# Performance work log

Hardware: AMD Instinct MI355X
Metric: run time of the kernel (lower is better)

## Reference

```python
import jax, jax.numpy as jnp
import numpy as np

ATT_LEN = 128  # must match init att_len


def setup_inputs() -> dict:
    key = jax.random.key(0)
    ks = jax.random.split(key, 6)
    B, T, U, L = 64, 4096, 512, ATT_LEN
    s = 1.0 / np.sqrt(U)
    return {
        "query": jax.random.normal(ks[0], (B, U), jnp.float32),
        "values": jax.random.normal(ks[1], (B, T, U), jnp.float32),
        "pos": jax.random.randint(ks[2], (B,), 0, T, jnp.int32),
        "W1": jax.random.normal(ks[3], (U, U), jnp.float32) * s,
        "b1": jnp.zeros((U,), jnp.float32),
        "W2": jax.random.normal(ks[4], (U, U), jnp.float32) * s,
        "b2": jnp.zeros((U,), jnp.float32),
        "V": jax.random.normal(ks[5], (U, 1), jnp.float32) * s,
        "bV": jnp.zeros((1,), jnp.float32),
    }


def _gather_windows(values, pos, att_len):
    """Vectorized version of the TF while_loop: per-example window of
    length att_len around pos, zero-padded where it runs off either end."""
    B, T, U = values.shape
    half = att_len // 2
    start = jnp.maximum(pos - half, 0)            # [B]
    end = jnp.minimum(pos + half, T)              # [B]
    xlen = end - start                            # [B]
    offs = jnp.arange(att_len, dtype=pos.dtype)   # [L]
    idx = start[:, None] + offs[None, :]          # [B, L]
    mask = offs[None, :] < xlen[:, None]          # [B, L] valid (unpadded) slots
    safe_idx = jnp.clip(idx, 0, T - 1)
    gathered = jnp.take_along_axis(values, safe_idx[:, :, None], axis=1)  # [B, L, U]
    values_att = jnp.where(mask[:, :, None], gathered, jnp.zeros((), values.dtype))
    xpos = jnp.where(mask, idx.astype(values.dtype), 0.0)  # [B, L]
    return values_att, xpos


def reference(query, values, pos, W1, b1, W2, b2, V, bV):
    values_att, _xpos = _gather_windows(values, pos, ATT_LEN)  # [B, L, U]
    # score = V(tanh(W1(values_att) + W2(query)[:, None, :]))
    h = jnp.tanh(jnp.einsum('blu,uv->blv', values_att, W1) + b1
                 + (query @ W2 + b2)[:, None, :])              # [B, L, U]
    score = jnp.einsum('blu,uo->blo', h, V) + bV               # [B, L, 1]
    attention_weights = jax.nn.softmax(score, axis=1)          # [B, L, 1]
    context_vector = jnp.sum(attention_weights * values_att, axis=1)  # [B, U]
    return context_vector, attention_weights
```

## Files before the change

kernel.cpp:

```cpp
#include <hip/hip_runtime.h>
#include <math.h>

#define NB 64
#define NT 4096
#define NU 512
#define NL 128
#define HALF 64

typedef __bf16 bf16x8 __attribute__((ext_vector_type(8)));
typedef float f32x4 __attribute__((ext_vector_type(4)));

__device__ inline unsigned short f2bf(float f) {
    unsigned u = __float_as_uint(f);
    u += 0x7fff + ((u >> 16) & 1);
    return (unsigned short)(u >> 16);
}

__device__ inline float tanh_fast(float x) {
    float xc = fminf(15.f, fmaxf(-15.f, x));
    float t = __expf(2.f * xc);
    return (t - 1.f) * __builtin_amdgcn_rcpf(t + 1.f);
}

__global__ __launch_bounds__(256) void k_prepA(const float* __restrict__ query,
                                               const float* __restrict__ values,
                                               const int* __restrict__ pos,
                                               const float* __restrict__ W1,
                                               const float* __restrict__ b1,
                                               const float* __restrict__ W2,
                                               const float* __restrict__ b2,
                                               float* __restrict__ q2,
                                               unsigned short* __restrict__ W1T,
                                               unsigned short* __restrict__ Gb) {
    __shared__ float sh[1056];
    const int blk = blockIdx.x, tid = threadIdx.x;

    if (blk < 256) {
        const int b = blk >> 2, cq = blk & 3;
        sh[tid]       = query[b * NU + tid];
        sh[tid + 256] = query[b * NU + tid + 256];
        __syncthreads();
        const int col  = cq * 128 + (tid & 127);
        const int half = tid >> 7;
        const float* wp = W2 + (size_t)(half * 256) * NU + col;
        float a = 0.f;
        #pragma unroll 8
        for (int uu = 0; uu < 256; ++uu)
            a = fmaf(sh[half * 256 + uu], wp[(size_t)uu * NU], a);
        if (half == 0) sh[512 + (tid & 127)] = a;
        __syncthreads();
        if (half == 1)
            q2[(size_t)b * NU + col] = a + sh[512 + (tid & 127)] + b1[col] + b2[col];
    } else if (blk < 512) {
        const int t  = blk - 256;
        const int tr = t >> 4, tc = t & 15;
        const int cc = tid & 31, r0 = tid >> 5;
        #pragma unroll
        for (int i = 0; i < 4; ++i) {
            const int r = r0 + i * 8;
            sh[r * 33 + cc] = W1[(size_t)(tr * 32 + r) * NU + tc * 32 + cc];
        }
        __syncthreads();
        #pragma unroll
        for (int i = 0; i < 4; ++i) {
            const int r = r0 + i * 8;
            W1T[(size_t)(tc * 32 + r) * NU + tr * 32 + cc] = f2bf(sh[cc * 33 + r]);
        }
    } else {
        const int g = blk - 512;
        #pragma unroll
        for (int i = 0; i < 8; ++i) {
            const int c   = tid + i * 256;
            const int rl  = c >> 7;
            const int off = (c & 127) * 4;
            const int rg  = g * 16 + rl;
            const int b   = rg >> 7, l = rg & 127;
            const int p     = pos[b];
            const int start = max(p - HALF, 0);
            const int xlen  = min(p + HALF, NT) - start;
            float4 v = make_float4(0.f, 0.f, 0.f, 0.f);
            if (l < xlen)
                v = *(const float4*)&values[((size_t)(b * NT + start + l)) * NU + off];
            uint2 pk;
            pk.x = f2bf(v.x) | ((unsigned)f2bf(v.y) << 16);
            pk.y = f2bf(v.z) | ((unsigned)f2bf(v.w) << 16);
            *(uint2*)&Gb[(size_t)rg * NU + off] = pk;
        }
    }
}

__global__ __launch_bounds__(256, 2) void k_score6(const unsigned short* __restrict__ Gb,
                                                   const unsigned short* __restrict__ W1T,
                                                   const float* __restrict__ q2,
                                                   const float* __restrict__ V,
                                                   float* __restrict__ part) {
    __shared__ unsigned short As[64 * 64];
    __shared__ unsigned short Bs[128 * 64];
    __shared__ float pl[64][2];

    const int id = blockIdx.x;
    const int nb = id >> 7, rb = id & 127;
    const int b  = rb >> 1, l0 = (rb & 1) * 64, n0 = nb * 128;
    const int tid = threadIdx.x, lane = tid & 63, w = tid >> 6;
    const int wr = w >> 1, wc = w & 1;

    const unsigned short* Asrc = Gb + ((size_t)(b * NL + l0)) * NU;
    const unsigned short* Bsrc = W1T + (size_t)n0 * NU;

    f32x4 acc[2][4];
    #pragma unroll
    for (int m = 0; m < 2; ++m)
        #pragma unroll
        for (int n = 0; n < 4; ++n) acc[m][n] = (f32x4){0.f, 0.f, 0.f, 0.f};

    for (int k0 = 0; k0 < NU; k0 += 64) {
        #pragma unroll
        for (int i = 0; i < 2; ++i) {
            const int c   = tid + i * 256;
            const int row = c >> 3, ch = c & 7;
            uint4 v = *(const uint4*)&Asrc[(size_t)row * NU + k0 + ch * 8];
            *(uint4*)((char*)As + row * 128 + ((ch * 16) ^ ((row & 7) << 4))) = v;
        }
        #pragma unroll
        for (int i = 0; i < 4; ++i) {
            const int c   = tid + i * 256;
            const int col = c >> 3, ch = c & 7;
            uint4 v = *(const uint4*)&Bsrc[(size_t)col * NU + k0 + ch * 8];
            *(uint4*)((char*)Bs + col * 128 + ((ch * 16) ^ ((col & 7) << 4))) = v;
        }
        __syncthreads();

        #pragma unroll
        for (int kh = 0; kh < 2; ++kh) {
            const int koff = kh * 64 + (lane >> 4) * 16;
            bf16x8 af[2];
            #pragma unroll
            for (int m = 0; m < 2; ++m) {
                const int rowA = wr * 32 + m * 16 + (lane & 15);
                af[m] = *(const bf16x8*)((const char*)As + rowA * 128 + (koff ^ ((rowA & 7) << 4)));
            }
            #pragma unroll
            for (int n = 0; n < 4; ++n) {
                const int colB = wc * 64 + n * 16 + (lane & 15);
                const bf16x8 bf = *(const bf16x8*)((const char*)Bs + colB * 128 + (koff ^ ((colB & 7) << 4)));
                #pragma unroll
                for (int m = 0; m < 2; ++m)
                    acc[m][n] = __builtin_amdgcn_mfma_f32_16x16x32_bf16(af[m], bf, acc[m][n], 0, 0, 0);
            }
        }
        __syncthreads();
    }

    float partial[2][4];
    #pragma unroll
    for (int m = 0; m < 2; ++m)
        #pragma unroll
        for (int r = 0; r < 4; ++r) partial[m][r] = 0.f;

    #pragma unroll
    for (int n = 0; n < 4; ++n) {
        const int col = n0 + wc * 64 + n * 16 + (lane & 15);
        const float qq = q2[(size_t)b * NU + col];
        const float vv = V[col];
        #pragma unroll
        for (int m = 0; m < 2; ++m)
            #pragma unroll
            for (int r = 0; r < 4; ++r)
                partial[m][r] += tanh_fast(acc[m][n][r] + qq) * vv;
    }
    #pragma unroll
    for (int off = 1; off < 16; off <<= 1)
        #pragma unroll
        for (int m = 0; m < 2; ++m)
            #pragma unroll
            for (int r = 0; r < 4; ++r)
                partial[m][r] += __shfl_xor(partial[m][r], off, 16);

    if ((lane & 15) == 0) {
        #pragma unroll
        for (int m = 0; m < 2; ++m)
            #pragma unroll
            for (int r = 0; r < 4; ++r)
                pl[wr * 32 + m * 16 + ((lane >> 4) << 2) + r][wc] = partial[m][r];
    }
    __syncthreads();

    if (tid < 64)
        part[((size_t)nb * NB + b) * NL + l0 + tid] = pl[tid][0] + pl[tid][1];
}

__global__ __launch_bounds__(256) void k_ctx2(const float* __restrict__ values,
                                              const int* __restrict__ pos,
                                              const float* __restrict__ part,
                                              const float* __restrict__ bV,
                                              float* __restrict__ out) {
    const int b = blockIdx.x, uq = blockIdx.y, tid = threadIdx.x;
    __shared__ float wsm[NL];
    __shared__ float red[4];
    __shared__ float cp[128];

    float s = -1e30f;
    if (tid < NL) {
        s = bV[0];
        #pragma unroll
        for (int nb = 0; nb < 4; ++nb) s += part[((size_t)nb * NB + b) * NL + tid];
    }
    float m = s;
    #pragma unroll
    for (int off = 32; off >= 1; off >>= 1) m = fmaxf(m, __shfl_xor(m, off, 64));
    if (tid < NL && (tid & 63) == 0) red[tid >> 6] = m;
    __syncthreads();
    const float M = fmaxf(red[0], red[1]);
    const float e = (tid < NL) ? __expf(s - M) : 0.f;
    float t = e;
    #pragma unroll
    for (int off = 32; off >= 1; off >>= 1) t += __shfl_xor(t, off, 64);
    if (tid < NL && (tid & 63) == 0) red[2 + (tid >> 6)] = t;
    __syncthreads();
    const float S = red[2] + red[3];
    if (tid < NL) {
        const float wv = e / S;
        wsm[tid] = wv;
        if (uq == 0) out[NB * NU + b * NL + tid] = wv;
    }
    __syncthreads();

    const int p     = pos[b];
    const int start = max(p - HALF, 0);
    const int xlen  = min(p + HALF, NT) - start;
    const float* vbase = values + ((size_t)b * NT + start) * NU;

    const int u    = uq * 128 + (tid & 127);
    const int half = tid >> 7;
    const int lbeg = half * 64;
    const int lend = min(xlen, lbeg + 64);
    float a = 0.f;
    #pragma unroll 4
    for (int l = lbeg; l < lend; ++l)
        a = fmaf(wsm[l], vbase[(size_t)l * NU + u], a);

    if (half == 0) cp[tid] = a;
    __syncthreads();
    if (half == 1) out[b * NU + u] = cp[tid & 127] + a;
}

#define BM 64
#define BN 128
#define BK 64
#define ASTRIDE 68

__global__ __launch_bounds__(256) void k_q2(const float* __restrict__ query,
                                            const float* __restrict__ W2,
                                            const float* __restrict__ b2,
                                            const float* __restrict__ b1,
                                            float* __restrict__ q2) {
    const int b = blockIdx.x, tid = threadIdx.x;
    __shared__ float qs[NU];
    qs[tid]       = query[b * NU + tid];
    qs[tid + 256] = query[b * NU + tid + 256];
    __syncthreads();
    float a0 = 0.f, a1 = 0.f;
    const float* w = W2 + tid;
    #pragma unroll 8
    for (int u = 0; u < NU; ++u) {
        const float q = qs[u];
        a0 = fmaf(q, w[(size_t)u * NU], a0);
        a1 = fmaf(q, w[(size_t)u * NU + 256], a1);
    }
    q2[b * NU + tid]       = a0 + b2[tid] + b1[tid];
    q2[b * NU + tid + 256] = a1 + b2[tid + 256] + b1[tid + 256];
}

__global__ __launch_bounds__(256) void k_score(const float* __restrict__ values,
                                               const int* __restrict__ pos,
                                               const float* __restrict__ W1,
                                               const float* __restrict__ V,
                                               const float* __restrict__ q2,
                                               float* __restrict__ part) {
    __shared__ float As2[BK][ASTRIDE];
    __shared__ float Bs2[BK][BN];
    const int rb = blockIdx.x, nb = blockIdx.y;
    const int b  = rb >> 1;
    const int l0 = (rb & 1) * BM;
    const int n0 = nb * BN;
    const int tid = threadIdx.x;
    const int tx = tid & 15, ty = tid >> 4;
    const int p     = pos[b];
    const int start = max(p - HALF, 0);
    const int xlen  = min(p + HALF, NT) - start;
    const float* vbase = values + ((size_t)b * NT + start) * NU;

    float acc[4][8];
    #pragma unroll
    for (int r = 0; r < 4; ++r)
        #pragma unroll
        for (int c = 0; c < 8; ++c) acc[r][c] = 0.f;

    for (int k0 = 0; k0 < NU; k0 += BK) {
        #pragma unroll
        for (int i = 0; i < 4; ++i) {
            const int f = tid + i * 256;
            const int row = f >> 4, kq = f & 15;
            const int l = l0 + row;
            float4 v4 = make_float4(0.f, 0.f, 0.f, 0.f);
            if (l < xlen)
                v4 = *(const float4*)&vbase[(size_t)l * NU + k0 + kq * 4];
            As2[kq * 4 + 0][row] = v4.x;
            As2[kq * 4 + 1][row] = v4.y;
            As2[kq * 4 + 2][row] = v4.z;
            As2[kq * 4 + 3][row] = v4.w;
        }
        #pragma unroll
        for (int i = 0; i < 8; ++i) {
            const int f = tid + i * 256;
            const int kk = f >> 5, nq = f & 31;
            *(float4*)&Bs2[kk][nq * 4] =
                *(const float4*)&W1[(size_t)(k0 + kk) * NU + n0 + nq * 4];
        }
        __syncthreads();
        #pragma unroll 16
        for (int kk = 0; kk < BK; ++kk) {
            const float4 a  = *(const float4*)&As2[kk][ty * 4];
            const float4 b0 = *(const float4*)&Bs2[kk][tx * 8];
            const float4 b1v = *(const float4*)&Bs2[kk][tx * 8 + 4];
            const float av[4] = {a.x, a.y, a.z, a.w};
            const float bv[8] = {b0.x, b0.y, b0.z, b0.w, b1v.x, b1v.y, b1v.z, b1v.w};
            #pragma unroll
            for (int r = 0; r < 4; ++r)
                #pragma unroll
                for (int c = 0; c < 8; ++c)
                    acc[r][c] = fmaf(av[r], bv[c], acc[r][c]);
        }
        __syncthreads();
    }
    float partial[4] = {0.f, 0.f, 0.f, 0.f};
    #pragma unroll
    for (int c = 0; c < 8; ++c) {
        const int v = n0 + tx * 8 + c;
        const float vv = V[v];
        const float qq = q2[b * NU + v];
        #pragma unroll
        for (int r = 0; r < 4; ++r)
            partial[r] += tanhf(acc[r][c] + qq) * vv;
    }
    #pragma unroll
    for (int off = 1; off < 16; off <<= 1)
        #pragma unroll
        for (int r = 0; r < 4; ++r)
            partial[r] += __shfl_xor(partial[r], off, 16);
    if (tx == 0) {
        #pragma unroll
        for (int r = 0; r < 4; ++r) {
            const int l = l0 + ty * 4 + r;
            part[((size_t)nb * NB + b) * NL + l] = partial[r];
        }
    }
}

__global__ __launch_bounds__(256) void k_ctx(const float* __restrict__ values,
                                             const int* __restrict__ pos,
                                             const float* __restrict__ part,
                                             const float* __restrict__ bV,
                                             float* __restrict__ out) {
    const int b = blockIdx.x, tid = threadIdx.x;
    __shared__ float wsh[NL];
    __shared__ float red2[4];

    float s = -1e30f;
    if (tid < NL) {
        s = bV[0];
        #pragma unroll
        for (int nb = 0; nb < 4; ++nb) s += part[((size_t)nb * NB + b) * NL + tid];
    }
    float m = s;
    #pragma unroll
    for (int off = 32; off >= 1; off >>= 1) m = fmaxf(m, __shfl_xor(m, off, 64));
    if (tid < NL && (tid & 63) == 0) red2[tid >> 6] = m;
    __syncthreads();
    const float M = fmaxf(red2[0], red2[1]);
    const float e = (tid < NL) ? expf(s - M) : 0.f;
    float t = e;
    #pragma unroll
    for (int off = 32; off >= 1; off >>= 1) t += __shfl_xor(t, off, 64);
    if (tid < NL && (tid & 63) == 0) red2[2 + (tid >> 6)] = t;
    __syncthreads();
    const float S = red2[2] + red2[3];
    if (tid < NL) wsh[tid] = e / S;
    __syncthreads();

    if (tid < NL) out[NB * NU + b * NL + tid] = wsh[tid];

    const int p     = pos[b];
    const int start = max(p - HALF, 0);
    const int xlen  = min(p + HALF, NT) - start;
    const float* vb = values + ((size_t)b * NT + start) * NU;

    float a0 = 0.f, a1 = 0.f;
    for (int l = 0; l < xlen; ++l) {
        const float wl = wsh[l];
        a0 = fmaf(wl, vb[(size_t)l * NU + tid], a0);
        a1 = fmaf(wl, vb[(size_t)l * NU + tid + 256], a1);
    }
    out[b * NU + tid]       = a0;
    out[b * NU + tid + 256] = a1;
}

extern "C" void kernel_launch(void* const* d_in, const int* in_sizes, int n_in,
                              void* d_out, int out_size, void* d_ws, size_t ws_size,
                              hipStream_t stream) {
    const float* query  = (const float*)d_in[0];
    const float* values = (const float*)d_in[1];
    const int*   pos    = (const int*)d_in[2];
    const float* W1     = (const float*)d_in[3];
    const float* b1     = (const float*)d_in[4];
    const float* W2     = (const float*)d_in[5];
    const float* b2     = (const float*)d_in[6];
    const float* V      = (const float*)d_in[7];
    const float* bV     = (const float*)d_in[8];
    float* out = (float*)d_out;

    const size_t need = 131072u + 131072u + 524288u + 8388608u;
    if (ws_size >= need) {
        float* q2            = (float*)d_ws;
        float* part          = (float*)((char*)d_ws + 131072);
        unsigned short* W1T  = (unsigned short*)((char*)d_ws + 262144);
        unsigned short* Gb   = (unsigned short*)((char*)d_ws + 786432);
        k_prepA<<<1024, 256, 0, stream>>>(query, values, pos, W1, b1, W2, b2, q2, W1T, Gb);
        k_score6<<<512, 256, 0, stream>>>(Gb, W1T, q2, V, part);
        k_ctx2<<<dim3(NB, 4), 256, 0, stream>>>(values, pos, part, bV, out);
    } else {
        float* q2   = (float*)d_ws;
        float* part = (float*)((char*)d_ws + 131072);
        k_q2<<<NB, 256, 0, stream>>>(query, W2, b2, b1, q2);
        k_score<<<dim3(NB * NL / BM, NU / BN), 256, 0, stream>>>(values, pos, W1, V, q2, part);
        k_ctx<<<NB, 256, 0, stream>>>(values, pos, part, bV, out);
    }
}
```

Measured before the change: 38.38 us.

## Fuse softmax/context into score kernel via last-block counter; use direct global-to-LDS loads

Removes the separate context kernel launch by having the last of the eight score blocks per batch (detected with an atomic counter reset in the prep kernel) compute the softmax and the weighted sum over values. Tile staging in the score GEMM now uses global_load_lds to write directly into LDS, with the swizzle moved to the source address. This saves a launch and the register round trip, but the final context work is done by a single block per batch, which serialises it into a tail of 64 blocks each walking 128 rows.

```diff
diff --git a/kernel.cpp b/kernel.cpp
--- a/kernel.cpp
+++ b/kernel.cpp
@@ -21,6 +21,11 @@
     float t = __expf(2.f * xc);
     return (t - 1.f) * __builtin_amdgcn_rcpf(t + 1.f);
 }
+
+#define GLL16(src, dst)                                                   \
+    __builtin_amdgcn_global_load_lds(                                     \
+        (const __attribute__((address_space(1))) void*)(src),             \
+        (__attribute__((address_space(3))) void*)(dst), 16, 0, 0)
 
 __global__ __launch_bounds__(256) void k_prepA(const float* __restrict__ query,
                                                const float* __restrict__ values,
@@ -31,7 +36,8 @@
                                                const float* __restrict__ b2,
                                                float* __restrict__ q2,
                                                unsigned short* __restrict__ W1T,
-                                               unsigned short* __restrict__ Gb) {
+                                               unsigned short* __restrict__ Gb,
+                                               int* __restrict__ cnt) {
     __shared__ float sh[1056];
     const int blk = blockIdx.x, tid = threadIdx.x;
 
@@ -67,6 +73,7 @@
             W1T[(size_t)(tc * 32 + r) * NU + tr * 32 + cc] = f2bf(sh[cc * 33 + r]);
         }
     } else {
+        if (blk == 512 && tid < NB) cnt[tid] = 0;
         const int g = blk - 512;
         #pragma unroll
         for (int i = 0; i < 8; ++i) {
@@ -89,14 +96,22 @@
     }
 }
 
-__global__ __launch_bounds__(256, 2) void k_score6(const unsigned short* __restrict__ Gb,
+__global__ __launch_bounds__(256, 2) void k_score7(const unsigned short* __restrict__ Gb,
                                                    const unsigned short* __restrict__ W1T,
                                                    const float* __restrict__ q2,
                                                    const float* __restrict__ V,
-                                                   float* __restrict__ part) {
+                                                   const float* __restrict__ values,
+                                                   const int* __restrict__ pos,
+                                                   const float* __restrict__ bV,
+                                                   float* __restrict__ part,
+                                                   int* __restrict__ cnt,
+                                                   float* __restrict__ out) {
     __shared__ unsigned short As[64 * 64];
     __shared__ unsigned short Bs[128 * 64];
     __shared__ float pl[64][2];
+    __shared__ float wsm[NL];
+    __shared__ float red[4];
+    __shared__ int amLastSh;
 
     const int id = blockIdx.x;
     const int nb = id >> 7, rb = id & 127;
@@ -118,15 +133,15 @@
         for (int i = 0; i < 2; ++i) {
             const int c   = tid + i * 256;
             const int row = c >> 3, ch = c & 7;
-            uint4 v = *(const uint4*)&Asrc[(size_t)row * NU + k0 + ch * 8];
-            *(uint4*)((char*)As + row * 128 + ((ch * 16) ^ ((row & 7) << 4))) = v;
+            GLL16(Asrc + (size_t)row * NU + k0 + ((ch ^ (row & 7)) * 8),
+                  (char*)As + c * 16);
         }
         #pragma unroll
         for (int i = 0; i < 4; ++i) {
             const int c   = tid + i * 256;
             const int col = c >> 3, ch = c & 7;
-            uint4 v = *(const uint4*)&Bsrc[(size_t)col * NU + k0 + ch * 8];
-            *(uint4*)((char*)Bs + col * 128 + ((ch * 16) ^ ((col & 7) << 4))) = v;
+            GLL16(Bsrc + (size_t)col * NU + k0 + ((ch ^ (col & 7)) * 8),
+                  (char*)Bs + c * 16);
         }
         __syncthreads();
 
@@ -185,25 +200,23 @@
     }
     __syncthreads();
 
-    if (tid < 64)
+    if (tid < 64) {
         part[((size_t)nb * NB + b) * NL + l0 + tid] = pl[tid][0] + pl[tid][1];
-}
-
-__global__ __launch_bounds__(256) void k_ctx2(const float* __restrict__ values,
-                                              const int* __restrict__ pos,
-                                              const float* __restrict__ part,
-                                              const float* __restrict__ bV,
-                                              float* __restrict__ out) {
-    const int b = blockIdx.x, uq = blockIdx.y, tid = threadIdx.x;
-    __shared__ float wsm[NL];
-    __shared__ float red[4];
-    __shared__ float cp[128];
+        __threadfence();
+    }
+    __syncthreads();
+    if (tid == 0)
+        amLastSh = (atomicAdd(&cnt[b], 1) == 7);
+    __syncthreads();
+    if (!amLastSh) return;
 
     float s = -1e30f;
     if (tid < NL) {
         s = bV[0];
         #pragma unroll
-        for (int nb = 0; nb < 4; ++nb) s += part[((size_t)nb * NB + b) * NL + tid];
+        for (int q = 0; q < 4; ++q)
+            s += __hip_atomic_load(&part[((size_t)q * NB + b) * NL + tid],
+                                   __ATOMIC_RELAXED, __HIP_MEMORY_SCOPE_AGENT);
     }
     float m = s;
     #pragma unroll
@@ -221,27 +234,23 @@
     if (tid < NL) {
         const float wv = e / S;
         wsm[tid] = wv;
-        if (uq == 0) out[NB * NU + b * NL + tid] = wv;
+        out[NB * NU + b * NL + tid] = wv;
     }
     __syncthreads();
 
     const int p     = pos[b];
     const int start = max(p - HALF, 0);
     const int xlen  = min(p + HALF, NT) - start;
-    const float* vbase = values + ((size_t)b * NT + start) * NU;
-
-    const int u    = uq * 128 + (tid & 127);
-    const int half = tid >> 7;
-    const int lbeg = half * 64;
-    const int lend = min(xlen, lbeg + 64);
-    float a = 0.f;
-    #pragma unroll 4
-    for (int l = lbeg; l < lend; ++l)
-        a = fmaf(wsm[l], vbase[(size_t)l * NU + u], a);
-
-    if (half == 0) cp[tid] = a;
-    __syncthreads();
-    if (half == 1) out[b * NU + u] = cp[tid & 127] + a;
+    const float* vb = values + ((size_t)b * NT + start) * NU;
+
+    float a0 = 0.f, a1 = 0.f;
+    for (int l = 0; l < xlen; ++l) {
+        const float wl = wsm[l];
+        a0 = fmaf(wl, vb[(size_t)l * NU + tid], a0);
+        a1 = fmaf(wl, vb[(size_t)l * NU + tid + 256], a1);
+    }
+    out[b * NU + tid]       = a0;
+    out[b * NU + tid + 256] = a1;
 }
 
 #define BM 64
@@ -419,15 +428,17 @@
     const float* bV     = (const float*)d_in[8];
     float* out = (float*)d_out;
 
-    const size_t need = 131072u + 131072u + 524288u + 8388608u;
+    const size_t need = 131072u + 131072u + 524288u + 8388608u + 256u;
     if (ws_size >= need) {
         float* q2            = (float*)d_ws;
         float* part          = (float*)((char*)d_ws + 131072);
         unsigned short* W1T  = (unsigned short*)((char*)d_ws + 262144);
         unsigned short* Gb   = (unsigned short*)((char*)d_ws + 786432);
-        k_prepA<<<1024, 256, 0, stream>>>(query, values, pos, W1, b1, W2, b2, q2, W1T, Gb);
-        k_score6<<<512, 256, 0, stream>>>(Gb, W1T, q2, V, part);
-        k_ctx2<<<dim3(NB, 4), 256, 0, stream>>>(values, pos, part, bV, out);
+        int* cnt             = (int*)((char*)d_ws + 786432 + 8388608);
+        k_prepA<<<1024, 256, 0, stream>>>(query, values, pos, W1, b1, W2, b2,
+                                          q2, W1T, Gb, cnt);
+        k_score7<<<512, 256, 0, stream>>>(Gb, W1T, q2, V, values, pos, bV,
+                                          part, cnt, out);
     } else {
         float* q2   = (float*)d_ws;
         float* part = (float*)((char*)d_ws + 131072);
```

Measured after the change: 44.79 us. +16.7%, slower.

## Double-buffer score GEMM tiles using direct global-to-LDS loads

Applied to the files above, without the earlier changes.

Switches the score GEMM's shared-memory staging from register round-trips to global_load_lds direct copies. The XOR swizzle moves from the LDS write address to the global read address. LDS is double-buffered so the next k-tile's load is issued before the MFMA work on the current tile, with one barrier per iteration. This aims to hide global load latency and save VGPRs and instructions, at the cost of doubling LDS use, which may limit occupancy. There is no explicit vmcnt wait before the barrier, so correctness depends on how the compiler orders the async LDS loads.

```diff
diff --git a/kernel.cpp b/kernel.cpp
--- a/kernel.cpp
+++ b/kernel.cpp
@@ -21,6 +21,11 @@
     float t = __expf(2.f * xc);
     return (t - 1.f) * __builtin_amdgcn_rcpf(t + 1.f);
 }
+
+#define GLL16(src, dst)                                                   \
+    __builtin_amdgcn_global_load_lds(                                     \
+        (const __attribute__((address_space(1))) void*)(src),             \
+        (__attribute__((address_space(3))) void*)(dst), 16, 0, 0)
 
 __global__ __launch_bounds__(256) void k_prepA(const float* __restrict__ query,
                                                const float* __restrict__ values,
@@ -89,13 +94,13 @@
     }
 }
 
-__global__ __launch_bounds__(256, 2) void k_score6(const unsigned short* __restrict__ Gb,
+__global__ __launch_bounds__(256, 2) void k_score8(const unsigned short* __restrict__ Gb,
                                                    const unsigned short* __restrict__ W1T,
                                                    const float* __restrict__ q2,
                                                    const float* __restrict__ V,
                                                    float* __restrict__ part) {
-    __shared__ unsigned short As[64 * 64];
-    __shared__ unsigned short Bs[128 * 64];
+    __shared__ unsigned short As[2][64 * 64];
+    __shared__ unsigned short Bs[2][128 * 64];
     __shared__ float pl[64][2];
 
     const int id = blockIdx.x;
@@ -113,22 +118,29 @@
         #pragma unroll
         for (int n = 0; n < 4; ++n) acc[m][n] = (f32x4){0.f, 0.f, 0.f, 0.f};
 
-    for (int k0 = 0; k0 < NU; k0 += 64) {
+    auto STAGE = [&](int buf, int k0) {
         #pragma unroll
         for (int i = 0; i < 2; ++i) {
-            const int c   = tid + i * 256;
+            const int c = tid + i * 256;
             const int row = c >> 3, ch = c & 7;
-            uint4 v = *(const uint4*)&Asrc[(size_t)row * NU + k0 + ch * 8];
-            *(uint4*)((char*)As + row * 128 + ((ch * 16) ^ ((row & 7) << 4))) = v;
+            GLL16(Asrc + (size_t)row * NU + k0 + ((ch ^ (row & 7)) * 8),
+                  (char*)As[buf] + c * 16);
         }
         #pragma unroll
         for (int i = 0; i < 4; ++i) {
-            const int c   = tid + i * 256;
+            const int c = tid + i * 256;
             const int col = c >> 3, ch = c & 7;
-            uint4 v = *(const uint4*)&Bsrc[(size_t)col * NU + k0 + ch * 8];
-            *(uint4*)((char*)Bs + col * 128 + ((ch * 16) ^ ((col & 7) << 4))) = v;
-        }
-        __syncthreads();
+            GLL16(Bsrc + (size_t)col * NU + k0 + ((ch ^ (col & 7)) * 8),
+                  (char*)Bs[buf] + c * 16);
+        }
+    };
+
+    STAGE(0, 0);
+    __syncthreads();
+
+    int cur = 0;
+    for (int t = 0; t < 8; ++t) {
+        if (t < 7) STAGE(cur ^ 1, (t + 1) * 64);
 
         #pragma unroll
         for (int kh = 0; kh < 2; ++kh) {
@@ -137,18 +149,19 @@
             #pragma unroll
             for (int m = 0; m < 2; ++m) {
                 const int rowA = wr * 32 + m * 16 + (lane & 15);
-                af[m] = *(const bf16x8*)((const char*)As + rowA * 128 + (koff ^ ((rowA & 7) << 4)));
+                af[m] = *(const bf16x8*)((const char*)As[cur] + rowA * 128 + (koff ^ ((rowA & 7) << 4)));
             }
             #pragma unroll
             for (int n = 0; n < 4; ++n) {
                 const int colB = wc * 64 + n * 16 + (lane & 15);
-                const bf16x8 bf = *(const bf16x8*)((const char*)Bs + colB * 128 + (koff ^ ((colB & 7) << 4)));
+                const bf16x8 bf = *(const bf16x8*)((const char*)Bs[cur] + colB * 128 + (koff ^ ((colB & 7) << 4)));
                 #pragma unroll
                 for (int m = 0; m < 2; ++m)
                     acc[m][n] = __builtin_amdgcn_mfma_f32_16x16x32_bf16(af[m], bf, acc[m][n], 0, 0, 0);
             }
         }
         __syncthreads();
+        cur ^= 1;
     }
 
     float partial[2][4];
@@ -426,7 +439,7 @@
         unsigned short* W1T  = (unsigned short*)((char*)d_ws + 262144);
         unsigned short* Gb   = (unsigned short*)((char*)d_ws + 786432);
         k_prepA<<<1024, 256, 0, stream>>>(query, values, pos, W1, b1, W2, b2, q2, W1T, Gb);
-        k_score6<<<512, 256, 0, stream>>>(Gb, W1T, q2, V, part);
+        k_score8<<<512, 256, 0, stream>>>(Gb, W1T, q2, V, part);
         k_ctx2<<<dim3(NB, 4), 256, 0, stream>>>(values, pos, part, bV, out);
     } else {
         float* q2   = (float*)d_ws;
```

Result: slower. 39.60 us (+3.2%).

## Fuse window gather and bf16 conversion into score GEMM tile loads

Applied to the files above, without the earlier changes.

The separate prep pass that gathered each window of values, converted it to bf16 and stored an 8 MB staging buffer is removed. The score kernel now reads fp32 values directly from the window, zero-pads rows past the valid length, and converts to bf16 while filling the LDS A tile. This removes a write and re-read of the staging buffer and one set of prep blocks, but each of the four N-blocks now reads fp32 values, twice the bytes of the bf16 copy, and does the conversion again. Block indices are also remapped so that the four N-blocks sharing one row tile land on the same XCD, which aims to improve L2 reuse of those reads.

```diff
diff --git a/kernel.cpp b/kernel.cpp
--- a/kernel.cpp
+++ b/kernel.cpp
@@ -22,16 +22,13 @@
     return (t - 1.f) * __builtin_amdgcn_rcpf(t + 1.f);
 }
 
-__global__ __launch_bounds__(256) void k_prepA(const float* __restrict__ query,
-                                               const float* __restrict__ values,
-                                               const int* __restrict__ pos,
+__global__ __launch_bounds__(256) void k_prepB(const float* __restrict__ query,
                                                const float* __restrict__ W1,
                                                const float* __restrict__ b1,
                                                const float* __restrict__ W2,
                                                const float* __restrict__ b2,
                                                float* __restrict__ q2,
-                                               unsigned short* __restrict__ W1T,
-                                               unsigned short* __restrict__ Gb) {
+                                               unsigned short* __restrict__ W1T) {
     __shared__ float sh[1056];
     const int blk = blockIdx.x, tid = threadIdx.x;
 
@@ -51,7 +48,7 @@
         __syncthreads();
         if (half == 1)
             q2[(size_t)b * NU + col] = a + sh[512 + (tid & 127)] + b1[col] + b2[col];
-    } else if (blk < 512) {
+    } else {
         const int t  = blk - 256;
         const int tr = t >> 4, tc = t & 15;
         const int cc = tid & 31, r0 = tid >> 5;
@@ -66,30 +63,11 @@
             const int r = r0 + i * 8;
             W1T[(size_t)(tc * 32 + r) * NU + tr * 32 + cc] = f2bf(sh[cc * 33 + r]);
         }
-    } else {
-        const int g = blk - 512;
-        #pragma unroll
-        for (int i = 0; i < 8; ++i) {
-            const int c   = tid + i * 256;
-            const int rl  = c >> 7;
-            const int off = (c & 127) * 4;
-            const int rg  = g * 16 + rl;
-            const int b   = rg >> 7, l = rg & 127;
-            const int p     = pos[b];
-            const int start = max(p - HALF, 0);
-            const int xlen  = min(p + HALF, NT) - start;
-            float4 v = make_float4(0.f, 0.f, 0.f, 0.f);
-            if (l < xlen)
-                v = *(const float4*)&values[((size_t)(b * NT + start + l)) * NU + off];
-            uint2 pk;
-            pk.x = f2bf(v.x) | ((unsigned)f2bf(v.y) << 16);
-            pk.y = f2bf(v.z) | ((unsigned)f2bf(v.w) << 16);
-            *(uint2*)&Gb[(size_t)rg * NU + off] = pk;
-        }
-    }
-}
-
-__global__ __launch_bounds__(256, 2) void k_score6(const unsigned short* __restrict__ Gb,
+    }
+}
+
+__global__ __launch_bounds__(256, 2) void k_score9(const float* __restrict__ values,
+                                                   const int* __restrict__ pos,
                                                    const unsigned short* __restrict__ W1T,
                                                    const float* __restrict__ q2,
                                                    const float* __restrict__ V,
@@ -98,13 +76,19 @@
     __shared__ unsigned short Bs[128 * 64];
     __shared__ float pl[64][2];
 
-    const int id = blockIdx.x;
-    const int nb = id >> 7, rb = id & 127;
-    const int b  = rb >> 1, l0 = (rb & 1) * 64, n0 = nb * 128;
+    const int id  = blockIdx.x;
+    const int xcd = id & 7, grp = id >> 3;
+    const int rb  = (grp >> 2) * 8 + xcd;
+    const int nb  = grp & 3;
+    const int b   = rb >> 1, l0 = (rb & 1) * 64, n0 = nb * 128;
     const int tid = threadIdx.x, lane = tid & 63, w = tid >> 6;
     const int wr = w >> 1, wc = w & 1;
 
-    const unsigned short* Asrc = Gb + ((size_t)(b * NL + l0)) * NU;
+    const int p     = pos[b];
+    const int start = max(p - HALF, 0);
+    const int xlen  = min(p + HALF, NT) - start;
+    const int xrem  = xlen - l0;
+    const float* vbase = values + ((size_t)(b * NT + start) + l0) * NU;
     const unsigned short* Bsrc = W1T + (size_t)n0 * NU;
 
     f32x4 acc[2][4];
@@ -115,11 +99,16 @@
 
     for (int k0 = 0; k0 < NU; k0 += 64) {
         #pragma unroll
-        for (int i = 0; i < 2; ++i) {
+        for (int i = 0; i < 4; ++i) {
             const int c   = tid + i * 256;
-            const int row = c >> 3, ch = c & 7;
-            uint4 v = *(const uint4*)&Asrc[(size_t)row * NU + k0 + ch * 8];
-            *(uint4*)((char*)As + row * 128 + ((ch * 16) ^ ((row & 7) << 4))) = v;
+            const int row = c >> 4, kq = c & 15;
+            float4 v = make_float4(0.f, 0.f, 0.f, 0.f);
+            if (row < xrem)
+                v = *(const float4*)&vbase[(size_t)row * NU + k0 + kq * 4];
+            uint2 pk;
+            pk.x = f2bf(v.x) | ((unsigned)f2bf(v.y) << 16);
+            pk.y = f2bf(v.z) | ((unsigned)f2bf(v.w) << 16);
+            *(uint2*)((char*)As + row * 128 + ((kq * 8) ^ ((row & 7) << 4))) = pk;
         }
         #pragma unroll
         for (int i = 0; i < 4; ++i) {
@@ -419,14 +408,12 @@
     const float* bV     = (const float*)d_in[8];
     float* out = (float*)d_out;
 
-    const size_t need = 131072u + 131072u + 524288u + 8388608u;
-    if (ws_size >= need) {
+    if (ws_size >= 786432u) {
         float* q2            = (float*)d_ws;
         float* part          = (float*)((char*)d_ws + 131072);
         unsigned short* W1T  = (unsigned short*)((char*)d_ws + 262144);
-        unsigned short* Gb   = (unsigned short*)((char*)d_ws + 786432);
-        k_prepA<<<1024, 256, 0, stream>>>(query, values, pos, W1, b1, W2, b2, q2, W1T, Gb);
-        k_score6<<<512, 256, 0, stream>>>(Gb, W1T, q2, V, part);
+        k_prepB<<<512, 256, 0, stream>>>(query, W1, b1, W2, b2, q2, W1T);
+        k_score9<<<512, 256, 0, stream>>>(values, pos, W1T, q2, V, part);
         k_ctx2<<<dim3(NB, 4), 256, 0, stream>>>(values, pos, part, bV, out);
     } else {
         float* q2   = (float*)d_ws;
```

Measured after the change: 45.72 us. 19.1% more time.
